# Kernel tuning notes

Hardware: AMD Instinct MI355X
Metric: run time of the kernel (lower is better)

## Reference

```python
import jax, jax.numpy as jnp
import numpy as np

B, T, F, H = 16384, 200, 4, 10

def _uniform(key, shape, fan):
    bound = 1.0 / np.sqrt(fan)
    return jax.random.uniform(key, shape, jnp.float32, -bound, bound)

def setup_inputs() -> dict:
    key = jax.random.key(0)
    ks = jax.random.split(key, 12)
    x = jax.random.normal(ks[0], (B, T, F), jnp.float32)
    return {
        "x": x,
        # layer 0 (input_size=4 -> hidden=10)
        "W_ih0": _uniform(ks[1], (H, F), H),
        "W_hh0": _uniform(ks[2], (H, H), H),
        "b_ih0": _uniform(ks[3], (H,), H),
        "b_hh0": _uniform(ks[4], (H,), H),
        # layer 1 (hidden=10 -> hidden=10)
        "W_ih1": _uniform(ks[5], (H, H), H),
        "W_hh1": _uniform(ks[6], (H, H), H),
        "b_ih1": _uniform(ks[7], (H,), H),
        "b_hh1": _uniform(ks[8], (H,), H),
        # fc head: Linear(hidden*seq_len -> 1) + sigmoid
        "W_fc": _uniform(ks[9], (1, H * T), H * T),
        "b_fc": _uniform(ks[10], (1,), H * T),
    }

def reference(x, W_ih0, W_hh0, b_ih0, b_hh0, W_ih1, W_hh1, b_ih1, b_hh1, W_fc, b_fc):
    Bv = x.shape[0]
    Hv = W_hh0.shape[0]
    # precompute input projection of layer 0 for all timesteps: [B,T,H]
    xp = jnp.einsum('btf,hf->bth', x, W_ih0) + b_ih0 + b_hh0

    def step(carry, xt):
        h0, h1 = carry
        h0 = jnp.tanh(xt + h0 @ W_hh0.T)                              # layer 0
        h1 = jnp.tanh(h0 @ W_ih1.T + b_ih1 + h1 @ W_hh1.T + b_hh1)   # layer 1
        return (h0, h1), h1

    h_init = (jnp.zeros((Bv, Hv), x.dtype), jnp.zeros((Bv, Hv), x.dtype))
    _, ys = jax.lax.scan(step, h_init, jnp.swapaxes(xp, 0, 1))  # ys: [T,B,H]
    out = jnp.swapaxes(ys, 0, 1).reshape(Bv, -1)                # [B, T*H], batch_first reshape
    return jax.nn.sigmoid(out @ W_fc.T + b_fc)                  # [B, 1]
```

## Files before the change

### kernel.cpp

```cpp
#include <hip/hip_runtime.h>
#include <math.h>

namespace {

constexpr int Bsz   = 16384;
constexpr int T     = 200;
constexpr int F     = 4;
constexpr int H     = 10;
constexpr int HP    = 16;
constexpr int BLOCK = 64;

__device__ __forceinline__ float fast_tanh(float x) {
  float e = exp2f(x * 2.8853900817779268f);
  return 1.0f - 2.0f * __builtin_amdgcn_rcpf(e + 1.0f);
}

__device__ __forceinline__ float fast_sigmoid(float x) {
  float e = exp2f(x * -1.4426950408889634f);
  return __builtin_amdgcn_rcpf(1.0f + e);
}

template <int J>
__device__ __forceinline__ float bcast8(float v) {
  return __int_as_float(
      __builtin_amdgcn_ds_swizzle(__float_as_int(v), (J << 5) | 0x18));
}

#define PIN(v) asm volatile("" : "+v"(v))

__global__ __launch_bounds__(BLOCK, 2) void rnn2_oct64(
    const float* __restrict__ x,
    const float* __restrict__ W_ih0, const float* __restrict__ W_hh0,
    const float* __restrict__ b_ih0, const float* __restrict__ b_hh0,
    const float* __restrict__ W_ih1, const float* __restrict__ W_hh1,
    const float* __restrict__ b_ih1, const float* __restrict__ b_hh1,
    const float* __restrict__ W_fc, const float* __restrict__ b_fc,
    float* __restrict__ out) {
  __shared__ float s_wfc[T * HP];
  for (int i = threadIdx.x; i < T * HP; i += BLOCK) {
    int t = i >> 4, u = i & 15;
    s_wfc[i] = (u < H) ? W_fc[t * H + u] : 0.0f;
  }
  __syncthreads();

  const int g  = blockIdx.x * BLOCK + threadIdx.x;
  const int b  = g >> 3;
  const int r  = g & 7;
  const int uA = r;
  const int uB = 8 + r;
  const bool vB = (uB < H);

  float wi0A[F], wh0A[H], wi1A[H], wh1A[H];
  float wi0B[F], wh0B[H], wi1B[H], wh1B[H];
  float bA0, bA1, bB0, bB1;
#pragma unroll
  for (int j = 0; j < F; ++j) {
    wi0A[j] = W_ih0[uA * F + j];              PIN(wi0A[j]);
    wi0B[j] = vB ? W_ih0[uB * F + j] : 0.0f;  PIN(wi0B[j]);
  }
#pragma unroll
  for (int j = 0; j < H; ++j) {
    wh0A[j] = W_hh0[uA * H + j];              PIN(wh0A[j]);
    wh0B[j] = vB ? W_hh0[uB * H + j] : 0.0f;  PIN(wh0B[j]);
    wi1A[j] = W_ih1[uA * H + j];              PIN(wi1A[j]);
    wi1B[j] = vB ? W_ih1[uB * H + j] : 0.0f;  PIN(wi1B[j]);
    wh1A[j] = W_hh1[uA * H + j];              PIN(wh1A[j]);
    wh1B[j] = vB ? W_hh1[uB * H + j] : 0.0f;  PIN(wh1B[j]);
  }
  bA0 = b_ih0[uA] + b_hh0[uA];               PIN(bA0);
  bB0 = vB ? (b_ih0[uB] + b_hh0[uB]) : 0.0f; PIN(bB0);
  bA1 = b_ih1[uA] + b_hh1[uA];               PIN(bA1);
  bB1 = vB ? (b_ih1[uB] + b_hh1[uB]) : 0.0f; PIN(bB1);

  const float4* __restrict__ xrow =
      reinterpret_cast<const float4*>(x + (size_t)b * (T * F));

  float h0b[H], h1b[H];
#pragma unroll
  for (int j = 0; j < H; ++j) { h0b[j] = 0.0f; h1b[j] = 0.0f; }
  float acc = 0.0f;

  float4 xv = xrow[0];
#pragma unroll 1
  for (int t = 0; t < T; ++t) {
    float4 xn = (t + 1 < T) ? xrow[t + 1] : xv;

    float fA = s_wfc[t * HP + uA];
    float fB = s_wfc[t * HP + uB];

    float sA = bA0, sB = bB0;
    sA = fmaf(wi0A[0], xv.x, sA);  sB = fmaf(wi0B[0], xv.x, sB);
    sA = fmaf(wi0A[1], xv.y, sA);  sB = fmaf(wi0B[1], xv.y, sB);
    sA = fmaf(wi0A[2], xv.z, sA);  sB = fmaf(wi0B[2], xv.z, sB);
    sA = fmaf(wi0A[3], xv.w, sA);  sB = fmaf(wi0B[3], xv.w, sB);
#pragma unroll
    for (int j = 0; j < H; ++j) {
      sA = fmaf(wh0A[j], h0b[j], sA);
      sB = fmaf(wh0B[j], h0b[j], sB);
    }
    float mA = fast_tanh(sA), mB = fast_tanh(sB);

    float pA = bA1, pB = bB1;
#pragma unroll
    for (int j = 0; j < H; ++j) {
      pA = fmaf(wh1A[j], h1b[j], pA);
      pB = fmaf(wh1B[j], h1b[j], pB);
    }

    h0b[0] = bcast8<0>(mA); h0b[1] = bcast8<1>(mA);
    h0b[2] = bcast8<2>(mA); h0b[3] = bcast8<3>(mA);
    h0b[4] = bcast8<4>(mA); h0b[5] = bcast8<5>(mA);
    h0b[6] = bcast8<6>(mA); h0b[7] = bcast8<7>(mA);
    h0b[8] = bcast8<0>(mB); h0b[9] = bcast8<1>(mB);

#pragma unroll
    for (int j = 0; j < H; ++j) {
      pA = fmaf(wi1A[j], h0b[j], pA);
      pB = fmaf(wi1B[j], h0b[j], pB);
    }
    mA = fast_tanh(pA); mB = fast_tanh(pB);

    acc = fmaf(mA, fA, acc);
    acc = fmaf(mB, fB, acc);

    h1b[0] = bcast8<0>(mA); h1b[1] = bcast8<1>(mA);
    h1b[2] = bcast8<2>(mA); h1b[3] = bcast8<3>(mA);
    h1b[4] = bcast8<4>(mA); h1b[5] = bcast8<5>(mA);
    h1b[6] = bcast8<6>(mA); h1b[7] = bcast8<7>(mA);
    h1b[8] = bcast8<0>(mB); h1b[9] = bcast8<1>(mB);

    xv = xn;
  }

  acc += __shfl_xor(acc, 1);
  acc += __shfl_xor(acc, 2);
  acc += __shfl_xor(acc, 4);
  if (r == 0) out[b] = fast_sigmoid(acc + b_fc[0]);
}

}

extern "C" void kernel_launch(void* const* d_in, const int* in_sizes, int n_in,
                              void* d_out, int out_size, void* d_ws, size_t ws_size,
                              hipStream_t stream) {
  const float* x     = (const float*)d_in[0];
  const float* W_ih0 = (const float*)d_in[1];
  const float* W_hh0 = (const float*)d_in[2];
  const float* b_ih0 = (const float*)d_in[3];
  const float* b_hh0 = (const float*)d_in[4];
  const float* W_ih1 = (const float*)d_in[5];
  const float* W_hh1 = (const float*)d_in[6];
  const float* b_ih1 = (const float*)d_in[7];
  const float* b_hh1 = (const float*)d_in[8];
  const float* W_fc  = (const float*)d_in[9];
  const float* b_fc  = (const float*)d_in[10];
  float* out = (float*)d_out;

  dim3 grid((Bsz * 8) / BLOCK), block(BLOCK);
  hipLaunchKernelGGL(rnn2_oct64, grid, block, 0, stream,
                     x, W_ih0, W_hh0, b_ih0, b_hh0,
                     W_ih1, W_hh1, b_ih1, b_hh1, W_fc, b_fc, out);
}
```

Baseline: 117.7 us.

## Process two batch elements per 8-lane group to reuse register weights and add ILP

```diff
diff --git a/kernel.cpp b/kernel.cpp
--- a/kernel.cpp
+++ b/kernel.cpp
@@ -28,7 +28,7 @@
 
 #define PIN(v) asm volatile("" : "+v"(v))
 
-__global__ __launch_bounds__(BLOCK, 2) void rnn2_oct64(
+__global__ __launch_bounds__(BLOCK, 1) void rnn2_oct_x2(
     const float* __restrict__ x,
     const float* __restrict__ W_ih0, const float* __restrict__ W_hh0,
     const float* __restrict__ b_ih0, const float* __restrict__ b_hh0,
@@ -43,99 +43,123 @@
   }
   __syncthreads();
 
-  const int g  = blockIdx.x * BLOCK + threadIdx.x;
-  const int b  = g >> 3;
-  const int r  = g & 7;
-  const int uA = r;
-  const int uB = 8 + r;
-  const bool vB = (uB < H);
+  const int lane = threadIdx.x;
+  const int grp  = lane >> 3;
+  const int r    = lane & 7;
+  const int ea   = blockIdx.x * 16 + grp * 2;
+  const int eb   = ea + 1;
+  const int uU = r;
+  const int uV = 8 + r;
+  const bool vV = (uV < H);
 
-  float wi0A[F], wh0A[H], wi1A[H], wh1A[H];
-  float wi0B[F], wh0B[H], wi1B[H], wh1B[H];
-  float bA0, bA1, bB0, bB1;
+  float wi0U[F], wh0U[H], wi1U[H], wh1U[H];
+  float wi0V[F], wh0V[H], wi1V[H], wh1V[H];
+  float bU0, bU1, bV0, bV1;
 #pragma unroll
   for (int j = 0; j < F; ++j) {
-    wi0A[j] = W_ih0[uA * F + j];              PIN(wi0A[j]);
-    wi0B[j] = vB ? W_ih0[uB * F + j] : 0.0f;  PIN(wi0B[j]);
+    wi0U[j] = W_ih0[uU * F + j];              PIN(wi0U[j]);
+    wi0V[j] = vV ? W_ih0[uV * F + j] : 0.0f;  PIN(wi0V[j]);
   }
 #pragma unroll
   for (int j = 0; j < H; ++j) {
-    wh0A[j] = W_hh0[uA * H + j];              PIN(wh0A[j]);
-    wh0B[j] = vB ? W_hh0[uB * H + j] : 0.0f;  PIN(wh0B[j]);
-    wi1A[j] = W_ih1[uA * H + j];              PIN(wi1A[j]);
-    wi1B[j] = vB ? W_ih1[uB * H + j] : 0.0f;  PIN(wi1B[j]);
-    wh1A[j] = W_hh1[uA * H + j];              PIN(wh1A[j]);
-    wh1B[j] = vB ? W_hh1[uB * H + j] : 0.0f;  PIN(wh1B[j]);
+    wh0U[j] = W_hh0[uU * H + j];              PIN(wh0U[j]);
+    wh0V[j] = vV ? W_hh0[uV * H + j] : 0.0f;  PIN(wh0V[j]);
+    wi1U[j] = W_ih1[uU * H + j];              PIN(wi1U[j]);
+    wi1V[j] = vV ? W_ih1[uV * H + j] : 0.0f;  PIN(wi1V[j]);
+    wh1U[j] = W_hh1[uU * H + j];              PIN(wh1U[j]);
+    wh1V[j] = vV ? W_hh1[uV * H + j] : 0.0f;  PIN(wh1V[j]);
   }
-  bA0 = b_ih0[uA] + b_hh0[uA];               PIN(bA0);
-  bB0 = vB ? (b_ih0[uB] + b_hh0[uB]) : 0.0f; PIN(bB0);
-  bA1 = b_ih1[uA] + b_hh1[uA];               PIN(bA1);
-  bB1 = vB ? (b_ih1[uB] + b_hh1[uB]) : 0.0f; PIN(bB1);
+  bU0 = b_ih0[uU] + b_hh0[uU];               PIN(bU0);
+  bV0 = vV ? (b_ih0[uV] + b_hh0[uV]) : 0.0f; PIN(bV0);
+  bU1 = b_ih1[uU] + b_hh1[uU];               PIN(bU1);
+  bV1 = vV ? (b_ih1[uV] + b_hh1[uV]) : 0.0f; PIN(bV1);
 
-  const float4* __restrict__ xrow =
-      reinterpret_cast<const float4*>(x + (size_t)b * (T * F));
+  const float4* __restrict__ xra =
+      reinterpret_cast<const float4*>(x + (size_t)ea * (T * F));
+  const float4* __restrict__ xrb =
+      reinterpret_cast<const float4*>(x + (size_t)eb * (T * F));
 
-  float h0b[H], h1b[H];
+  float h0a[H], h1a[H], h0b[H], h1b[H];
 #pragma unroll
-  for (int j = 0; j < H; ++j) { h0b[j] = 0.0f; h1b[j] = 0.0f; }
-  float acc = 0.0f;
+  for (int j = 0; j < H; ++j) { h0a[j] = h1a[j] = h0b[j] = h1b[j] = 0.0f; }
+  float acca = 0.0f, accb = 0.0f;
 
-  float4 xv = xrow[0];
+  float4 xa = xra[0], xb = xrb[0];
 #pragma unroll 1
   for (int t = 0; t < T; ++t) {
-    float4 xn = (t + 1 < T) ? xrow[t + 1] : xv;
+    float4 xna = (t + 1 < T) ? xra[t + 1] : xa;
+    float4 xnb = (t + 1 < T) ? xrb[t + 1] : xb;
 
-    float fA = s_wfc[t * HP + uA];
-    float fB = s_wfc[t * HP + uB];
+    float fU = s_wfc[t * HP + uU];
+    float fV = s_wfc[t * HP + uV];
 
-    float sA = bA0, sB = bB0;
-    sA = fmaf(wi0A[0], xv.x, sA);  sB = fmaf(wi0B[0], xv.x, sB);
-    sA = fmaf(wi0A[1], xv.y, sA);  sB = fmaf(wi0B[1], xv.y, sB);
-    sA = fmaf(wi0A[2], xv.z, sA);  sB = fmaf(wi0B[2], xv.z, sB);
-    sA = fmaf(wi0A[3], xv.w, sA);  sB = fmaf(wi0B[3], xv.w, sB);
+    float sUa = bU0, sVa = bV0, sUb = bU0, sVb = bV0;
+    sUa = fmaf(wi0U[0], xa.x, sUa);  sUb = fmaf(wi0U[0], xb.x, sUb);
+    sVa = fmaf(wi0V[0], xa.x, sVa);  sVb = fmaf(wi0V[0], xb.x, sVb);
+    sUa = fmaf(wi0U[1], xa.y, sUa);  sUb = fmaf(wi0U[1], xb.y, sUb);
+    sVa = fmaf(wi0V[1], xa.y, sVa);  sVb = fmaf(wi0V[1], xb.y, sVb);
+    sUa = fmaf(wi0U[2], xa.z, sUa);  sUb = fmaf(wi0U[2], xb.z, sUb);
+    sVa = fmaf(wi0V[2], xa.z, sVa);  sVb = fmaf(wi0V[2], xb.z, sVb);
+    sUa = fmaf(wi0U[3], xa.w, sUa);  sUb = fmaf(wi0U[3], xb.w, sUb);
+    sVa = fmaf(wi0V[3], xa.w, sVa);  sVb = fmaf(wi0V[3], xb.w, sVb);
 #pragma unroll
     for (int j = 0; j < H; ++j) {
-      sA = fmaf(wh0A[j], h0b[j], sA);
-      sB = fmaf(wh0B[j], h0b[j], sB);
+      sUa = fmaf(wh0U[j], h0a[j], sUa);  sUb = fmaf(wh0U[j], h0b[j], sUb);
+      sVa = fmaf(wh0V[j], h0a[j], sVa);  sVb = fmaf(wh0V[j], h0b[j], sVb);
     }
-    float mA = fast_tanh(sA), mB = fast_tanh(sB);
+    float mUa = fast_tanh(sUa), mVa = fast_tanh(sVa);
+    float mUb = fast_tanh(sUb), mVb = fast_tanh(sVb);
 
-    float pA = bA1, pB = bB1;
+    h0a[0] = bcast8<0>(mUa); h0a[1] = bcast8<1>(mUa);
+    h0a[2] = bcast8<2>(mUa); h0a[3] = bcast8<3>(mUa);
+    h0a[4] = bcast8<4>(mUa); h0a[5] = bcast8<5>(mUa);
+    h0a[6] = bcast8<6>(mUa); h0a[7] = bcast8<7>(mUa);
+    h0a[8] = bcast8<0>(mVa); h0a[9] = bcast8<1>(mVa);
+    h0b[0] = bcast8<0>(mUb); h0b[1] = bcast8<1>(mUb);
+    h0b[2] = bcast8<2>(mUb); h0b[3] = bcast8<3>(mUb);
+    h0b[4] = bcast8<4>(mUb); h0b[5] = bcast8<5>(mUb);
+    h0b[6] = bcast8<6>(mUb); h0b[7] = bcast8<7>(mUb);
+    h0b[8] = bcast8<0>(mVb); h0b[9] = bcast8<1>(mVb);
+
+    float pUa = bU1, pVa = bV1, pUb = bU1, pVb = bV1;
 #pragma unroll
     for (int j = 0; j < H; ++j) {
-      pA = fmaf(wh1A[j], h1b[j], pA);
-      pB = fmaf(wh1B[j], h1b[j], pB);
+      pUa = fmaf(wh1U[j], h1a[j], pUa);  pUb = fmaf(wh1U[j], h1b[j], pUb);
+      pVa = fmaf(wh1V[j], h1a[j], pVa);  pVb = fmaf(wh1V[j], h1b[j], pVb);
     }
-
-    h0b[0] = bcast8<0>(mA); h0b[1] = bcast8<1>(mA);
-    h0b[2] = bcast8<2>(mA); h0b[3] = bcast8<3>(mA);
-    h0b[4] = bcast8<4>(mA); h0b[5] = bcast8<5>(mA);
-    h0b[6] = bcast8<6>(mA); h0b[7] = bcast8<7>(mA);
-    h0b[8] = bcast8<0>(mB); h0b[9] = bcast8<1>(mB);
 
 #pragma unroll
     for (int j = 0; j < H; ++j) {
-      pA = fmaf(wi1A[j], h0b[j], pA);
-      pB = fmaf(wi1B[j], h0b[j], pB);
+      pUa = fmaf(wi1U[j], h0a[j], pUa);  pUb = fmaf(wi1U[j], h0b[j], pUb);
+      pVa = fmaf(wi1V[j], h0a[j], pVa);  pVb = fmaf(wi1V[j], h0b[j], pVb);
     }
-    mA = fast_tanh(pA); mB = fast_tanh(pB);
+    mUa = fast_tanh(pUa); mVa = fast_tanh(pVa);
+    mUb = fast_tanh(pUb); mVb = fast_tanh(pVb);
 
-    acc = fmaf(mA, fA, acc);
-    acc = fmaf(mB, fB, acc);
+    acca = fmaf(mUa, fU, acca);  accb = fmaf(mUb, fU, accb);
+    acca = fmaf(mVa, fV, acca);  accb = fmaf(mVb, fV, accb);
 
-    h1b[0] = bcast8<0>(mA); h1b[1] = bcast8<1>(mA);
-    h1b[2] = bcast8<2>(mA); h1b[3] = bcast8<3>(mA);
-    h1b[4] = bcast8<4>(mA); h1b[5] = bcast8<5>(mA);
-    h1b[6] = bcast8<6>(mA); h1b[7] = bcast8<7>(mA);
-    h1b[8] = bcast8<0>(mB); h1b[9] = bcast8<1>(mB);
+    h1a[0] = bcast8<0>(mUa); h1a[1] = bcast8<1>(mUa);
+    h1a[2] = bcast8<2>(mUa); h1a[3] = bcast8<3>(mUa);
+    h1a[4] = bcast8<4>(mUa); h1a[5] = bcast8<5>(mUa);
+    h1a[6] = bcast8<6>(mUa); h1a[7] = bcast8<7>(mUa);
+    h1a[8] = bcast8<0>(mVa); h1a[9] = bcast8<1>(mVa);
+    h1b[0] = bcast8<0>(mUb); h1b[1] = bcast8<1>(mUb);
+    h1b[2] = bcast8<2>(mUb); h1b[3] = bcast8<3>(mUb);
+    h1b[4] = bcast8<4>(mUb); h1b[5] = bcast8<5>(mUb);
+    h1b[6] = bcast8<6>(mUb); h1b[7] = bcast8<7>(mUb);
+    h1b[8] = bcast8<0>(mVb); h1b[9] = bcast8<1>(mVb);
 
-    xv = xn;
+    xa = xna; xb = xnb;
   }
 
-  acc += __shfl_xor(acc, 1);
-  acc += __shfl_xor(acc, 2);
-  acc += __shfl_xor(acc, 4);
-  if (r == 0) out[b] = fast_sigmoid(acc + b_fc[0]);
+  acca += __shfl_xor(acca, 1);  accb += __shfl_xor(accb, 1);
+  acca += __shfl_xor(acca, 2);  accb += __shfl_xor(accb, 2);
+  acca += __shfl_xor(acca, 4);  accb += __shfl_xor(accb, 4);
+  if (r == 0) {
+    out[ea] = fast_sigmoid(acca + b_fc[0]);
+    out[eb] = fast_sigmoid(accb + b_fc[0]);
+  }
 }
 
 }
@@ -156,8 +180,8 @@
   const float* b_fc  = (const float*)d_in[10];
   float* out = (float*)d_out;
 
-  dim3 grid((Bsz * 8) / BLOCK), block(BLOCK);
-  hipLaunchKernelGGL(rnn2_oct64, grid, block, 0, stream,
+  dim3 grid(Bsz / 16), block(BLOCK);
+  hipLaunchKernelGGL(rnn2_oct_x2, grid, block, 0, stream,
                      x, W_ih0, W_hh0, b_ih0, b_hh0,
                      W_ih1, W_hh1, b_ih1, b_hh1, W_fc, b_fc, out);
 }
```

After: 158.2 us. 34.4% more time.
